# Kernel optimization log

Measured on AMD Instinct MI355X. Metric: run time of the kernel, lower is better.

Reference implementation:

```python
import jax, jax.numpy as jnp
import numpy as np

BN_EPS = 1e-5
LEAKY_SLOPE = 0.1


def setup_inputs() -> dict:
    key = jax.random.key(0)
    ks = jax.random.split(key, 4)
    b, c, h, w = 4, 64, 64, 64
    exemplar = jax.random.normal(ks[0], (b, c, h, w), dtype=jnp.float32)
    query = jax.random.normal(ks[1], (b, c, h, w), dtype=jnp.float32)
    W_lin = jax.random.normal(ks[2], (c, c), dtype=jnp.float32) * (1.0 / np.sqrt(c))
    W_conv = jax.random.normal(ks[3], (c, c, 3, 3), dtype=jnp.float32) * (1.0 / np.sqrt(c * 9))
    gamma = jnp.ones((c,), dtype=jnp.float32)
    beta = jnp.zeros((c,), dtype=jnp.float32)
    return {"exemplar": exemplar, "query": query, "W_lin": W_lin,
            "W_conv": W_conv, "gamma": gamma, "beta": beta}


def reference(exemplar, query, W_lin, W_conv, gamma, beta):
    b, c, h, w = exemplar.shape
    hw = h * w
    ex_flat = exemplar.reshape(b, c, hw)          # [b, C, hw]
    q_flat = query.reshape(b, c, hw)              # [b, C, hw]
    # linear_e on transposed exemplar: [b, hw, C] @ W_lin.T
    ex_l = jnp.einsum('bnc,oc->bno', ex_flat.transpose(0, 2, 1), W_lin)
    # affinity A: [b, hw, hw]
    A = jnp.einsum('bnc,bcm->bnm', ex_l, q_flat)
    # B = softmax(A^T, dim=1); C = softmax(A, dim=1)
    Bmat = jax.nn.softmax(A.transpose(0, 2, 1), axis=1)
    Cmat = jax.nn.softmax(A, axis=1)
    query_c = jnp.einsum('bcm,bmn->bcn', q_flat, Bmat)     # [b, C, hw]
    exemplar_c = jnp.einsum('bcm,bmn->bcn', ex_flat, Cmat)  # [b, C, hw]
    out_x = (exemplar_c + query_c).reshape(b, c, h, w) + exemplar + query
    # conv3x3 (no bias) -> batchnorm (training-mode batch stats) -> leaky relu
    y = jax.lax.conv_general_dilated(
        out_x, W_conv, window_strides=(1, 1), padding=[(1, 1), (1, 1)],
        dimension_numbers=('NCHW', 'OIHW', 'NCHW'))
    mean = jnp.mean(y, axis=(0, 2, 3), keepdims=True)
    var = jnp.mean((y - mean) ** 2, axis=(0, 2, 3), keepdims=True)
    y = (y - mean) * jax.lax.rsqrt(var + BN_EPS)
    y = y * gamma[None, :, None, None] + beta[None, :, None, None]
    return jnp.where(y > 0, y, LEAKY_SLOPE * y)
```

## Files before the change

kernel.cpp:

```cpp
#include <hip/hip_runtime.h>


typedef short bf16x8 __attribute__((ext_vector_type(8)));
typedef float f32x4 __attribute__((ext_vector_type(4)));
typedef unsigned int u32x4 __attribute__((ext_vector_type(4)));
typedef unsigned short ushort_t;
typedef ushort_t ushort8 __attribute__((ext_vector_type(8)));

#define HW 4096
#define NC 64
#define NB 4
#define RT_L2E 1.2011224087864498f

#define GLB(p) ((const __attribute__((address_space(1))) unsigned int*)(p))
#define LDSP(p) ((__attribute__((address_space(3))) unsigned int*)(p))

__device__ __forceinline__ ushort_t f2bf(float f) {
  unsigned u = __builtin_bit_cast(unsigned, f);
  unsigned r = u + 0x7FFFu + ((u >> 16) & 1u);
  return (ushort_t)(r >> 16);
}

__device__ __forceinline__ float bf2f(ushort_t u) {
  unsigned v = ((unsigned)u) << 16;
  return __builtin_bit_cast(float, v);
}

__device__ __forceinline__ float fast_exp2(float x) {
#if __has_builtin(__builtin_amdgcn_exp2f)
  return __builtin_amdgcn_exp2f(x);
#else
  return exp2f(x);
#endif
}

__device__ __forceinline__ unsigned cvt_pk_bf16(float lo, float hi) {
  unsigned r;
  asm("v_cvt_pk_bf16_f32 %0, %1, %2" : "=v"(r) : "v"(lo), "v"(hi));
  return r;
}

__global__ __launch_bounds__(256) void prep_kernel(
    const float* __restrict__ ex, const float* __restrict__ q,
    const float* __restrict__ Wl, const float* __restrict__ Wc,
    ushort_t* __restrict__ exlT_s, ushort_t* __restrict__ qT_s,
    ushort_t* __restrict__ q_tl, ushort_t* __restrict__ ex_tl,
    ushort_t* __restrict__ exq, ushort_t* __restrict__ w9f)
{
  __shared__ float exs[64][33];
  __shared__ float wls[64][64];

  const int t = threadIdx.x;
  const int b = blockIdx.x >> 7;
  const int chunk = blockIdx.x & 127;
  const int g = t >> 5;
  const int p = t & 31;
  const int pos = chunk * 32 + p;
  const int tile = pos >> 6;
  const int kv = pos & 63;
  const int vcol = ((kv >> 5) << 5) + (((kv >> 2) & 3) << 3)
                 + (((kv >> 4) & 1) << 2) + (kv & 3);

  {
    int widx = blockIdx.x * 256 + t;
    if (widx < 36864) {
      int o   = widx / 576;
      int rem = widx - o * 576;
      int c   = rem / 9;
      int tap = rem - c * 9;
      w9f[tap * 4096 + o * 64 + c] = f2bf(Wc[widx]);
    }
  }

  const float* exb = ex + (size_t)b * NC * HW;
  const float* qb  = q  + (size_t)b * NC * HW;
  ushort_t* exlTsb = exlT_s+ (size_t)b * HW * NC;
  ushort_t* qTsb   = qT_s  + (size_t)b * HW * NC;
  ushort_t* exqb   = exq   + (size_t)b * HW * NC;
  ushort_t* qtlb   = q_tl  + (size_t)b * HW * NC + (size_t)tile * 4096 + vcol;
  ushort_t* etlb   = ex_tl + (size_t)b * HW * NC + (size_t)tile * 4096 + vcol;

#pragma unroll
  for (int it = 0; it < 16; ++it) {
    int idx = it * 256 + t;
    wls[idx >> 6][idx & 63] = Wl[idx];
  }

  ushort8 qhs, eqh;
#pragma unroll
  for (int j = 0; j < 8; ++j) {
    int c = g * 8 + j;
    float ev = exb[c * HW + pos];
    exs[c][p] = ev;
    etlb[c * 64] = f2bf(ev);
    float qv = qb[c * HW + pos];
    qtlb[c * 64] = f2bf(qv);
    qhs[j] = f2bf(qv * RT_L2E);
    eqh[j] = f2bf(ev + qv);
  }
  *(ushort8*)(qTsb + (size_t)pos * NC + g * 8) = qhs;
  *(ushort8*)(exqb + (size_t)pos * NC + g * 8) = eqh;
  __syncthreads();

  float acc[8];
#pragma unroll
  for (int oo = 0; oo < 8; ++oo) acc[oo] = 0.f;
  for (int c = 0; c < 64; ++c) {
    float xv = exs[c][p];
#pragma unroll
    for (int oo = 0; oo < 8; ++oo)
      acc[oo] += wls[g * 8 + oo][c] * xv;
  }
  {
    ushort8 hs;
#pragma unroll
    for (int oo = 0; oo < 8; ++oo) hs[oo] = f2bf(acc[oo] * RT_L2E);
    *(ushort8*)(exlTsb + (size_t)pos * NC + g * 8) = hs;
  }
}

__global__ __launch_bounds__(512) void attn_kernel(
    const ushort_t* __restrict__ exlT_s, const ushort_t* __restrict__ qT_s,
    const ushort_t* __restrict__ q_tl, const ushort_t* __restrict__ ex_tl,
    ushort_t* __restrict__ Opart, float* __restrict__ lpart, int ss)
{
  __shared__ char smem[32768];

  const int gid  = blockIdx.x;
  const int S    = 1 << ss;
  const int kvs  = gid & (S - 1);
  const int qb   = (gid >> ss) & 31;
  const int b    = (gid >> (ss + 5)) & 3;
  const int pass = gid >> (ss + 7);
  const int w    = threadIdx.x >> 6;
  const int lane = threadIdx.x & 63;
  const int lr = lane & 15, lg = lane >> 4;
  const int qrow0 = qb * 128 + w * 16;

  const ushort_t* QT = (pass ? qT_s : exlT_s) + (size_t)b * HW * NC;
  const ushort_t* KT = (pass ? exlT_s : qT_s) + (size_t)b * HW * NC;
  const ushort_t* VT = (pass ? ex_tl : q_tl) + (size_t)b * HW * NC;

  bf16x8 aq[2];
  {
    const ushort_t* qp = QT + (size_t)(qrow0 + lr) * NC + lg * 8;
    aq[0] = *(const bf16x8*)(qp);
    aq[1] = *(const bf16x8*)(qp + 32);
  }

  const u32x4 onesu = {0x3F803F80u, 0x3F803F80u, 0x3F803F80u, 0x3F803F80u};
  const bf16x8 vones = __builtin_bit_cast(bf16x8, onesu);

  f32x4 O[4];
  f32x4 lacc = (f32x4){0.f, 0.f, 0.f, 0.f};
#pragma unroll
  for (int t = 0; t < 4; ++t) O[t] = (f32x4){0.f, 0.f, 0.f, 0.f};

  const int niter = 64 >> ss;
  const int kv0 = kvs * niter;

  const int db0 = w * 1024 + (lane << 4);
#define STAGE(phase, kvb)                                                      \
  {                                                                            \
    char* Kl = smem + (phase) * 16384;                                         \
    char* Vl = Kl + 8192;                                                      \
    const char* kg = (const char*)(KT + (size_t)(kvb) * 64 * NC);              \
    const char* vg = (const char*)(VT + (size_t)(kvb) * 4096);                 \
    int swz = db0 ^ (((db0 >> 7) & 7) << 4);                                   \
    __builtin_amdgcn_global_load_lds(GLB(kg + swz),                            \
                                     LDSP(Kl + w * 1024), 16, 0, 0);           \
    __builtin_amdgcn_global_load_lds(GLB(vg + swz),                            \
                                     LDSP(Vl + w * 1024), 16, 0, 0);           \
  }

  STAGE(0, kv0);
  __syncthreads();

  int cur = 0;
  for (int i = 0; i < niter; ++i) {
    if (i + 1 < niter) STAGE(cur ^ 1, kv0 + i + 1);

    const char* Kl = smem + cur * 16384;
    const char* Vl = Kl + 8192;
    const int cswz = (lr & 7) << 4;

    f32x4 s[4];
#pragma unroll
    for (int t = 0; t < 4; ++t) s[t] = (f32x4){0.f, 0.f, 0.f, 0.f};
#pragma unroll
    for (int ks = 0; ks < 2; ++ks)
#pragma unroll
      for (int t = 0; t < 4; ++t) {
        bf16x8 kf = *(const bf16x8*)(Kl + (t * 16 + lr) * 128
                                     + ((ks * 64 + lg * 16) ^ cswz));
        s[t] = __builtin_amdgcn_mfma_f32_16x16x32_bf16(kf, aq[ks], s[t], 0, 0, 0);
      }

    unsigned int pa[2][4];
#pragma unroll
    for (int ks = 0; ks < 2; ++ks)
#pragma unroll
      for (int hf = 0; hf < 2; ++hf) {
        const int t = ks * 2 + hf;
        float p0 = fast_exp2(s[t][0]);
        float p1 = fast_exp2(s[t][1]);
        float p2 = fast_exp2(s[t][2]);
        float p3 = fast_exp2(s[t][3]);
        pa[ks][hf * 2]     = cvt_pk_bf16(p0, p1);
        pa[ks][hf * 2 + 1] = cvt_pk_bf16(p2, p3);
      }

#pragma unroll
    for (int ks = 0; ks < 2; ++ks) {
      u32x4 pv = {pa[ks][0], pa[ks][1], pa[ks][2], pa[ks][3]};
      bf16x8 paf = __builtin_bit_cast(bf16x8, pv);
      lacc = __builtin_amdgcn_mfma_f32_16x16x32_bf16(paf, vones, lacc, 0, 0, 0);
#pragma unroll
      for (int t = 0; t < 4; ++t) {
        bf16x8 vf = *(const bf16x8*)(Vl + (t * 16 + lr) * 128
                                     + ((ks * 64 + lg * 16) ^ cswz));
        O[t] = __builtin_amdgcn_mfma_f32_16x16x32_bf16(paf, vf, O[t], 0, 0, 0);
      }
    }

    __syncthreads();
    cur ^= 1;
  }

  ushort_t* Ob = Opart + ((size_t)((pass * 4 + b) * S + kvs)) * (HW * NC);
  float* lp = lpart + ((size_t)((pass * 4 + b) * S + kvs)) * HW;
#pragma unroll
  for (int t = 0; t < 4; ++t)
#pragma unroll
    for (int r = 0; r < 4; ++r)
      Ob[(size_t)(qrow0 + lg * 4 + r) * NC + t * 16 + lr] = f2bf(O[t][r]);
  if (lr == 0) {
#pragma unroll
    for (int r = 0; r < 4; ++r) lp[qrow0 + lg * 4 + r] = lacc[r];
  }
#undef STAGE
}

__global__ __launch_bounds__(256) void merge_kernel(
    const ushort_t* __restrict__ Opart, const float* __restrict__ lpart,
    const ushort_t* __restrict__ exq, ushort_t* __restrict__ xconv, int S)
{
  const int idx = blockIdx.x * 256 + threadIdx.x;
  const int c8  = (idx & 7) * 8;
  const int pos = (idx >> 3) & 4095;
  const int b   = idx >> 15;
  const int h   = pos >> 6;
  const int w   = pos & 63;

  float acc[8];
  {
    ushort8 e = *(const ushort8*)(exq + ((size_t)b * HW + pos) * NC + c8);
#pragma unroll
    for (int j = 0; j < 8; ++j) acc[j] = bf2f(e[j]);
  }

#pragma unroll
  for (int pass = 0; pass < 2; ++pass) {
    const int pp = pass * 4 + b;
    const ushort_t* opb = Opart + (size_t)pp * S * (HW * NC)
                        + (size_t)pos * NC + c8;
    float os[8];
#pragma unroll
    for (int j = 0; j < 8; ++j) os[j] = 0.f;
    float ls = 0.f;
    for (int s = 0; s < S; ++s) {
      ushort8 v = *(const ushort8*)(opb + (size_t)s * (HW * NC));
#pragma unroll
      for (int j = 0; j < 8; ++j) os[j] += bf2f(v[j]);
      ls += lpart[(size_t)(pp * S + s) * HW + pos];
    }
    float inv = 1.0f / ls;
#pragma unroll
    for (int j = 0; j < 8; ++j) acc[j] += os[j] * inv;
  }

  ushort_t* row = xconv + ((size_t)(b * 64 + h) * 66) * NC;
  ushort8 outv;
#pragma unroll
  for (int j = 0; j < 8; ++j) outv[j] = f2bf(acc[j]);
  *(ushort8*)(row + (size_t)(w + 1) * NC + c8) = outv;

  ushort8 z = {0, 0, 0, 0, 0, 0, 0, 0};
  if (w == 0)  *(ushort8*)(row + c8) = z;
  if (w == 63) *(ushort8*)(row + (size_t)65 * NC + c8) = z;
}

#define XSZ 25344
__global__ __launch_bounds__(256) void conv_kernel(
    const ushort_t* __restrict__ xconv, const ushort_t* __restrict__ w9f,
    float* __restrict__ y, float* __restrict__ pstats)
{
  __shared__ char smem[XSZ + 73728];
  const int t  = threadIdx.x;
  const int h  = blockIdx.x & 63;
  const int b  = blockIdx.x >> 6;
  const int wv = t >> 6;
  const int lane = t & 63;
  const int lr = lane & 15, lg = lane >> 4;

  {
    const char* wsrc = (const char*)w9f;
#pragma unroll
    for (int i = 0; i < 18; ++i) {
      int d = (i * 256 + t) * 16;
      int s = d ^ (((d >> 7) & 7) << 4);
      __builtin_amdgcn_global_load_lds(GLB(wsrc + s),
          LDSP(smem + XSZ + (i * 256 + wv * 64) * 16), 16, 0, 0);
    }
  }

#pragma unroll
  for (int ky = 0; ky < 3; ++ky) {
    const int hs = h + ky - 1;
    char* dst0 = smem + ky * 8448;
    if (hs >= 0 && hs < 64) {
      const char* src = (const char*)(xconv + (size_t)(b * 64 + hs) * 66 * NC);
#pragma unroll
      for (int i = 0; i < 2; ++i) {
        int d = (i * 256 + t) * 16;
        int s = d ^ (((d >> 7) & 7) << 4);
        __builtin_amdgcn_global_load_lds(GLB(src + s),
            LDSP(dst0 + (i * 256 + wv * 64) * 16), 16, 0, 0);
      }
      if (t < 16) {
        int d = (512 + t) * 16;
        int s = d ^ (((d >> 7) & 7) << 4);
        __builtin_amdgcn_global_load_lds(GLB(src + s),
            LDSP(dst0 + 512 * 16), 16, 0, 0);
      }
    } else {
      u32x4 z = {0, 0, 0, 0};
#pragma unroll
      for (int i = 0; i < 2; ++i)
        *(u32x4*)(dst0 + (i * 256 + t) * 16) = z;
      if (t < 16) *(u32x4*)(dst0 + (512 + t) * 16) = z;
    }
  }
  __syncthreads();

  const char* xls = smem;
  const char* wls = smem + XSZ;

  f32x4 O[4];
#pragma unroll
  for (int tt = 0; tt < 4; ++tt) O[tt] = (f32x4){0.f, 0.f, 0.f, 0.f};

  const int orow = wv * 16 + lr;
  const int oswz = (lr & 7) << 4;

#pragma unroll
  for (int tap = 0; tap < 9; ++tap) {
    const int ky = tap / 3, kx = tap % 3;
    bf16x8 wa[2];
#pragma unroll
    for (int ks = 0; ks < 2; ++ks)
      wa[ks] = *(const bf16x8*)(wls + tap * 8192 + orow * 128
                                + (((ks * 4 + lg) << 4) ^ oswz));
#pragma unroll
    for (int tt = 0; tt < 4; ++tt) {
      const int row = tt * 16 + lr + kx;
      const int rswz = (row & 7) << 4;
#pragma unroll
      for (int ks = 0; ks < 2; ++ks) {
        bf16x8 bf = *(const bf16x8*)(xls + ky * 8448 + row * 128
                                     + (((ks * 4 + lg) << 4) ^ rswz));
        O[tt] = __builtin_amdgcn_mfma_f32_16x16x32_bf16(wa[ks], bf, O[tt], 0, 0, 0);
      }
    }
  }

  float* ps = pstats + (size_t)blockIdx.x * 128;
#pragma unroll
  for (int r = 0; r < 4; ++r) {
    const int o = wv * 16 + lg * 4 + r;
    float s1 = 0.f, s2 = 0.f;
#pragma unroll
    for (int tt = 0; tt < 4; ++tt) {
      float v = O[tt][r];
      y[(size_t)(b * 64 + o) * HW + h * 64 + tt * 16 + lr] = v;
      s1 += v; s2 += v * v;
    }
    s1 += __shfl_xor(s1, 1); s1 += __shfl_xor(s1, 2);
    s1 += __shfl_xor(s1, 4); s1 += __shfl_xor(s1, 8);
    s2 += __shfl_xor(s2, 1); s2 += __shfl_xor(s2, 2);
    s2 += __shfl_xor(s2, 4); s2 += __shfl_xor(s2, 8);
    if (lr == 0) { ps[o] = s1; ps[64 + o] = s2; }
  }
}

__global__ __launch_bounds__(128) void statred_kernel(
    const float* __restrict__ pstats, float* __restrict__ stats)
{
  const int i = threadIdx.x;
  float s = 0.f;
  for (int k = 0; k < 256; ++k) s += pstats[k * 128 + i];
  stats[i] = s;
}

__global__ __launch_bounds__(256) void bn_kernel(
    const float* __restrict__ y, const float* __restrict__ stats,
    const float* __restrict__ gamma, const float* __restrict__ beta,
    float* __restrict__ out)
{
  const int e = (blockIdx.x * 256 + threadIdx.x) * 4;
  const int o = (e >> 12) & 63;
  float mean = stats[o] * (1.f / 16384.f);
  float var  = stats[64 + o] * (1.f / 16384.f) - mean * mean;
  float g  = gamma[o] * rsqrtf(var + 1e-5f);
  float bt = beta[o] - mean * g;
  float4 v = *(const float4*)(y + e);
  float4 r;
  r.x = v.x * g + bt; r.x = r.x > 0.f ? r.x : 0.1f * r.x;
  r.y = v.y * g + bt; r.y = r.y > 0.f ? r.y : 0.1f * r.y;
  r.z = v.z * g + bt; r.z = r.z > 0.f ? r.z : 0.1f * r.z;
  r.w = v.w * g + bt; r.w = r.w > 0.f ? r.w : 0.1f * r.w;
  *(float4*)(out + e) = r;
}

extern "C" void kernel_launch(void* const* d_in, const int* in_sizes, int n_in,
                              void* d_out, int out_size, void* d_ws, size_t ws_size,
                              hipStream_t stream)
{
  const float* ex    = (const float*)d_in[0];
  const float* q     = (const float*)d_in[1];
  const float* Wl    = (const float*)d_in[2];
  const float* Wc    = (const float*)d_in[3];
  const float* gamma = (const float*)d_in[4];
  const float* beta  = (const float*)d_in[5];
  float* out = (float*)d_out;

  char* ws = (char*)d_ws;
  ushort_t* exlT_s = (ushort_t*)(ws);
  ushort_t* qT_s   = (ushort_t*)(ws + (2u << 20));
  ushort_t* q_tl   = (ushort_t*)(ws + (4u << 20));
  ushort_t* ex_tl  = (ushort_t*)(ws + (6u << 20));
  ushort_t* exq    = (ushort_t*)(ws + (8u << 20));
  ushort_t* xconv  = (ushort_t*)(ws + (10u << 20));
  float* stats  = (float*)(ws + (14u << 20));
  float* lpart  = (float*)(ws + (14u << 20) + 65536);
  float* pstats = (float*)(ws + (14u << 20) + 589824);
  ushort_t* w9f = (ushort_t*)(ws + (14u << 20) + 786432);
  ushort_t* Opart = (ushort_t*)(ws + (15u << 20));
  float* yBuf  = (float*)(ws);

  int ss;
  if (ws_size >= (31u << 20)) ss = 2;
  else if (ws_size >= (23u << 20)) ss = 1;
  else ss = 0;
  const int S = 1 << ss;

  prep_kernel<<<512, 256, 0, stream>>>(ex, q, Wl, Wc, exlT_s, qT_s, q_tl, ex_tl,
                                       exq, w9f);
  attn_kernel<<<256 * S, 512, 0, stream>>>(exlT_s, qT_s, q_tl, ex_tl,
                                           Opart, lpart, ss);
  merge_kernel<<<512, 256, 0, stream>>>(Opart, lpart, exq, xconv, S);
  conv_kernel<<<256, 256, 0, stream>>>(xconv, w9f, yBuf, pstats);
  statred_kernel<<<1, 128, 0, stream>>>(pstats, stats);
  bn_kernel<<<1024, 256, 0, stream>>>(yBuf, stats, gamma, beta, out);
}
```

Baseline: 71.00 us.

## Process two 16-row query tiles per wave to reuse K/V LDS fragments

Each wave now handles 32 query rows instead of 16, so every K and V fragment read from LDS feeds two MFMAs. The query block grows to 256 rows and the grid is halved. A launch_bounds occupancy hint is added. This cuts LDS traffic and global K/V staging per query row, at the cost of more registers and fewer blocks (128*S) to spread across the CUs.

```diff
diff --git a/kernel.cpp b/kernel.cpp
--- a/kernel.cpp
+++ b/kernel.cpp
@@ -119,7 +119,7 @@
   }
 }
 
-__global__ __launch_bounds__(512) void attn_kernel(
+__global__ __launch_bounds__(512, 4) void attn_kernel(
     const ushort_t* __restrict__ exlT_s, const ushort_t* __restrict__ qT_s,
     const ushort_t* __restrict__ q_tl, const ushort_t* __restrict__ ex_tl,
     ushort_t* __restrict__ Opart, float* __restrict__ lpart, int ss)
@@ -129,32 +129,39 @@
   const int gid  = blockIdx.x;
   const int S    = 1 << ss;
   const int kvs  = gid & (S - 1);
-  const int qb   = (gid >> ss) & 31;
-  const int b    = (gid >> (ss + 5)) & 3;
-  const int pass = gid >> (ss + 7);
+  const int qb   = (gid >> ss) & 15;
+  const int b    = (gid >> (ss + 4)) & 3;
+  const int pass = gid >> (ss + 6);
   const int w    = threadIdx.x >> 6;
   const int lane = threadIdx.x & 63;
   const int lr = lane & 15, lg = lane >> 4;
-  const int qrow0 = qb * 128 + w * 16;
+  const int qrow0 = qb * 256 + w * 32;
 
   const ushort_t* QT = (pass ? qT_s : exlT_s) + (size_t)b * HW * NC;
   const ushort_t* KT = (pass ? exlT_s : qT_s) + (size_t)b * HW * NC;
   const ushort_t* VT = (pass ? ex_tl : q_tl) + (size_t)b * HW * NC;
 
-  bf16x8 aq[2];
+  bf16x8 aq0[2], aq1[2];
   {
-    const ushort_t* qp = QT + (size_t)(qrow0 + lr) * NC + lg * 8;
-    aq[0] = *(const bf16x8*)(qp);
-    aq[1] = *(const bf16x8*)(qp + 32);
+    const ushort_t* qp0 = QT + (size_t)(qrow0 + lr) * NC + lg * 8;
+    aq0[0] = *(const bf16x8*)(qp0);
+    aq0[1] = *(const bf16x8*)(qp0 + 32);
+    const ushort_t* qp1 = QT + (size_t)(qrow0 + 16 + lr) * NC + lg * 8;
+    aq1[0] = *(const bf16x8*)(qp1);
+    aq1[1] = *(const bf16x8*)(qp1 + 32);
   }
 
   const u32x4 onesu = {0x3F803F80u, 0x3F803F80u, 0x3F803F80u, 0x3F803F80u};
   const bf16x8 vones = __builtin_bit_cast(bf16x8, onesu);
 
-  f32x4 O[4];
-  f32x4 lacc = (f32x4){0.f, 0.f, 0.f, 0.f};
-#pragma unroll
-  for (int t = 0; t < 4; ++t) O[t] = (f32x4){0.f, 0.f, 0.f, 0.f};
+  f32x4 O0[4], O1[4];
+  f32x4 lacc0 = (f32x4){0.f, 0.f, 0.f, 0.f};
+  f32x4 lacc1 = (f32x4){0.f, 0.f, 0.f, 0.f};
+#pragma unroll
+  for (int t = 0; t < 4; ++t) {
+    O0[t] = (f32x4){0.f, 0.f, 0.f, 0.f};
+    O1[t] = (f32x4){0.f, 0.f, 0.f, 0.f};
+  }
 
   const int niter = 64 >> ss;
   const int kv0 = kvs * niter;
@@ -184,42 +191,56 @@
     const char* Vl = Kl + 8192;
     const int cswz = (lr & 7) << 4;
 
-    f32x4 s[4];
-#pragma unroll
-    for (int t = 0; t < 4; ++t) s[t] = (f32x4){0.f, 0.f, 0.f, 0.f};
+    f32x4 s0[4], s1[4];
+#pragma unroll
+    for (int t = 0; t < 4; ++t) {
+      s0[t] = (f32x4){0.f, 0.f, 0.f, 0.f};
+      s1[t] = (f32x4){0.f, 0.f, 0.f, 0.f};
+    }
 #pragma unroll
     for (int ks = 0; ks < 2; ++ks)
 #pragma unroll
       for (int t = 0; t < 4; ++t) {
         bf16x8 kf = *(const bf16x8*)(Kl + (t * 16 + lr) * 128
                                      + ((ks * 64 + lg * 16) ^ cswz));
-        s[t] = __builtin_amdgcn_mfma_f32_16x16x32_bf16(kf, aq[ks], s[t], 0, 0, 0);
-      }
-
-    unsigned int pa[2][4];
+        s0[t] = __builtin_amdgcn_mfma_f32_16x16x32_bf16(kf, aq0[ks], s0[t], 0, 0, 0);
+        s1[t] = __builtin_amdgcn_mfma_f32_16x16x32_bf16(kf, aq1[ks], s1[t], 0, 0, 0);
+      }
+
+    unsigned int pa0[2][4], pa1[2][4];
 #pragma unroll
     for (int ks = 0; ks < 2; ++ks)
 #pragma unroll
       for (int hf = 0; hf < 2; ++hf) {
         const int t = ks * 2 + hf;
-        float p0 = fast_exp2(s[t][0]);
-        float p1 = fast_exp2(s[t][1]);
-        float p2 = fast_exp2(s[t][2]);
-        float p3 = fast_exp2(s[t][3]);
-        pa[ks][hf * 2]     = cvt_pk_bf16(p0, p1);
-        pa[ks][hf * 2 + 1] = cvt_pk_bf16(p2, p3);
+        float a0 = fast_exp2(s0[t][0]);
+        float a1 = fast_exp2(s0[t][1]);
+        float a2 = fast_exp2(s0[t][2]);
+        float a3 = fast_exp2(s0[t][3]);
+        pa0[ks][hf * 2]     = cvt_pk_bf16(a0, a1);
+        pa0[ks][hf * 2 + 1] = cvt_pk_bf16(a2, a3);
+        float c0 = fast_exp2(s1[t][0]);
+        float c1 = fast_exp2(s1[t][1]);
+        float c2 = fast_exp2(s1[t][2]);
+        float c3 = fast_exp2(s1[t][3]);
+        pa1[ks][hf * 2]     = cvt_pk_bf16(c0, c1);
+        pa1[ks][hf * 2 + 1] = cvt_pk_bf16(c2, c3);
       }
 
 #pragma unroll
     for (int ks = 0; ks < 2; ++ks) {
-      u32x4 pv = {pa[ks][0], pa[ks][1], pa[ks][2], pa[ks][3]};
-      bf16x8 paf = __builtin_bit_cast(bf16x8, pv);
-      lacc = __builtin_amdgcn_mfma_f32_16x16x32_bf16(paf, vones, lacc, 0, 0, 0);
+      u32x4 pv0 = {pa0[ks][0], pa0[ks][1], pa0[ks][2], pa0[ks][3]};
+      u32x4 pv1 = {pa1[ks][0], pa1[ks][1], pa1[ks][2], pa1[ks][3]};
+      bf16x8 paf0 = __builtin_bit_cast(bf16x8, pv0);
+      bf16x8 paf1 = __builtin_bit_cast(bf16x8, pv1);
+      lacc0 = __builtin_amdgcn_mfma_f32_16x16x32_bf16(paf0, vones, lacc0, 0, 0, 0);
+      lacc1 = __builtin_amdgcn_mfma_f32_16x16x32_bf16(paf1, vones, lacc1, 0, 0, 0);
 #pragma unroll
       for (int t = 0; t < 4; ++t) {
         bf16x8 vf = *(const bf16x8*)(Vl + (t * 16 + lr) * 128
                                      + ((ks * 64 + lg * 16) ^ cswz));
-        O[t] = __builtin_amdgcn_mfma_f32_16x16x32_bf16(paf, vf, O[t], 0, 0, 0);
+        O0[t] = __builtin_amdgcn_mfma_f32_16x16x32_bf16(paf0, vf, O0[t], 0, 0, 0);
+        O1[t] = __builtin_amdgcn_mfma_f32_16x16x32_bf16(paf1, vf, O1[t], 0, 0, 0);
       }
     }
 
@@ -232,11 +253,16 @@
 #pragma unroll
   for (int t = 0; t < 4; ++t)
 #pragma unroll
-    for (int r = 0; r < 4; ++r)
-      Ob[(size_t)(qrow0 + lg * 4 + r) * NC + t * 16 + lr] = f2bf(O[t][r]);
+    for (int r = 0; r < 4; ++r) {
+      Ob[(size_t)(qrow0 + lg * 4 + r) * NC + t * 16 + lr] = f2bf(O0[t][r]);
+      Ob[(size_t)(qrow0 + 16 + lg * 4 + r) * NC + t * 16 + lr] = f2bf(O1[t][r]);
+    }
   if (lr == 0) {
 #pragma unroll
-    for (int r = 0; r < 4; ++r) lp[qrow0 + lg * 4 + r] = lacc[r];
+    for (int r = 0; r < 4; ++r) {
+      lp[qrow0 + lg * 4 + r] = lacc0[r];
+      lp[qrow0 + 16 + lg * 4 + r] = lacc1[r];
+    }
   }
 #undef STAGE
 }
@@ -456,7 +482,7 @@
 
   prep_kernel<<<512, 256, 0, stream>>>(ex, q, Wl, Wc, exlT_s, qT_s, q_tl, ex_tl,
                                        exq, w9f);
-  attn_kernel<<<256 * S, 512, 0, stream>>>(exlT_s, qT_s, q_tl, ex_tl,
+  attn_kernel<<<128 * S, 512, 0, stream>>>(exlT_s, qT_s, q_tl, ex_tl,
                                            Opart, lpart, ss);
   merge_kernel<<<512, 256, 0, stream>>>(Opart, lpart, exq, xconv, S);
   conv_kernel<<<256, 256, 0, stream>>>(xconv, w9f, yBuf, pstats);
```

Measured after the change: 67.98 us. 4.3% less time.
